# Kernel optimization log

Measured on AMD Instinct MI355X. Metric: run time of the kernel, lower is better.

The kernel has to match this reference:

```python
import jax, jax.numpy as jnp
import numpy as np

N, E, H = 1024, 2048, 32
DIMS = [4, 128, 512, 1028]
NEG_SLOPE_ATT = 0.2   # GATv2 attention LeakyReLU
NEG_SLOPE_ACT = 0.01  # torch.nn.LeakyReLU default


def _lin(key, fan_in, fan_out):
    k1, k2 = jax.random.split(key)
    s = 1.0 / np.sqrt(fan_in)
    return (jax.random.uniform(k1, (fan_in, fan_out), jnp.float32, -s, s),
            jax.random.uniform(k2, (fan_out,), jnp.float32, -s, s))


def setup_inputs() -> dict:
    key = jax.random.key(0)
    ks = jax.random.split(key, 32)
    inp = {
        'x': jax.random.normal(ks[0], (N, 4), jnp.float32),
        'edge_index': jax.random.randint(ks[1], (2, E), 0, N, jnp.int64),
    }
    # GATv2 layers: lin_l/lin_r -> heads*out, att [H, C], bias [C]
    ki = 2
    for i in range(3):
        cin, cout = DIMS[i], DIMS[i + 1]
        wl, bl = _lin(ks[ki], cin, H * cout); ki += 1
        wr, br = _lin(ks[ki], cin, H * cout); ki += 1
        att = jax.random.normal(ks[ki], (H, cout), jnp.float32) * 0.05; ki += 1
        bias = jnp.zeros((cout,), jnp.float32)
        j = i + 1
        inp.update({f'w{j}l': wl, f'b{j}l': bl, f'w{j}r': wr, f'b{j}r': br,
                    f'att{j}': att, f'gb{j}': bias})
    # decoder MLP 1028 -> 512 -> 128 -> 2
    for j, (cin, cout) in enumerate([(1028, 512), (512, 128), (128, 2)], 1):
        w, b = _lin(ks[ki], cin, cout); ki += 1
        inp[f'dw{j}'] = w
        inp[f'db{j}'] = b
    return inp


def _gatv2(x, src, dst, wl, bl, wr, br, att, bias, cout):
    # lin_l on source nodes, lin_r on target nodes (PyG GATv2Conv)
    xl = (x @ wl + bl).reshape(-1, H, cout)   # [N, H, C]
    xr = (x @ wr + br).reshape(-1, H, cout)
    e = jax.nn.leaky_relu(xl[src] + xr[dst], NEG_SLOPE_ATT)  # [Etot, H, C]
    score = jnp.einsum('ehc,hc->eh', e, att)                  # [Etot, H]
    smax = jax.ops.segment_max(score, dst, num_segments=N)
    alpha = jnp.exp(score - smax[dst])
    denom = jax.ops.segment_sum(alpha, dst, num_segments=N)
    alpha = alpha / denom[dst]
    out = jax.ops.segment_sum(alpha[:, :, None] * xl[src], dst, num_segments=N)
    return out.mean(axis=1) + bias  # concat=False: average heads


def reference(x, edge_index,
              w1l, b1l, w1r, b1r, att1, gb1,
              w2l, b2l, w2r, b2r, att2, gb2,
              w3l, b3l, w3r, b3r, att3, gb3,
              dw1, db1, dw2, db2, dw3, db3):
    # add self loops (PyG default)
    loop = jnp.arange(N, dtype=edge_index.dtype)
    src = jnp.concatenate([edge_index[0], loop])
    dst = jnp.concatenate([edge_index[1], loop])

    act = lambda z: jax.nn.leaky_relu(z, NEG_SLOPE_ACT)
    z = _gatv2(x, src, dst, w1l, b1l, w1r, b1r, att1, gb1, 128)
    z = act(z)
    z = _gatv2(z, src, dst, w2l, b2l, w2r, b2r, att2, gb2, 512)
    z = act(z)
    z = _gatv2(z, src, dst, w3l, b3l, w3r, b3r, att3, gb3, 1028)

    z = act(z @ dw1 + db1)
    z = act(z @ dw2 + db2)
    z = z @ dw3 + db3  # [N, 2]
    return z.reshape(-1)
```

## Files before the change

kernel.cpp:

```cpp
#include <hip/hip_runtime.h>
#include <cstdint>
#include <cstddef>

#define NN 1024
#define EE 2048
#define ETOT 3072
#define HH 32

typedef __bf16 bf16_t;
typedef __attribute__((ext_vector_type(8))) __bf16 bf16x8;
typedef __attribute__((ext_vector_type(4))) __bf16 bf16x4;
typedef __attribute__((ext_vector_type(2))) __bf16 bf16x2;
typedef __attribute__((ext_vector_type(4))) float f32x4;

typedef const __attribute__((address_space(1))) void gvoid_t;
typedef __attribute__((address_space(3))) void lvoid_t;

__device__ __forceinline__ void gll16(const void* g, void* l) {
    __builtin_amdgcn_global_load_lds((gvoid_t*)g, (lvoid_t*)l, 16, 0, 0);
}

__global__ void k_zero_int(int* p, int n) {
    int i = blockIdx.x * 256 + threadIdx.x;
    if (i < n) p[i] = 0;
}

__global__ void k_detect(const int* ei, int* flag) {
    int i = blockIdx.x * 256 + threadIdx.x;
    int idx = 2 * i + 1;
    if (idx < 2 * EE && ei[idx] != 0) atomicOr(flag, 1);
}

__global__ void k_edge_prep(const int* ei, const int* flag, int* srcA, int* dstA, int* cnt) {
    int e = blockIdx.x * 256 + threadIdx.x;
    if (e >= ETOT) return;
    int s, d;
    if (e < EE) {
        if (*flag) { s = ei[e]; d = ei[EE + e]; }
        else       { s = ei[2 * e]; d = ei[2 * (EE + e)]; }
        s &= (NN - 1); d &= (NN - 1);
    } else {
        s = d = e - EE;
    }
    srcA[e] = s; dstA[e] = d;
    atomicAdd(&cnt[d], 1);
}

__global__ void k_scan(const int* cnt, int* off) {
    __shared__ int sh[NN];
    int t = threadIdx.x;
    sh[t] = cnt[t];
    __syncthreads();
    for (int o = 1; o < NN; o <<= 1) {
        int v = (t >= o) ? sh[t - o] : 0;
        __syncthreads();
        sh[t] += v;
        __syncthreads();
    }
    off[t + 1] = sh[t];
    if (t == 0) off[0] = 0;
}

__global__ void k_fill(const int* dstA, const int* off, int* cur, int* csre) {
    int e = blockIdx.x * 256 + threadIdx.x;
    if (e >= ETOT) return;
    int d = dstA[e];
    int p = atomicAdd(&cur[d], 1);
    csre[off[d] + p] = e;
}

__global__ void k_convA(const float* __restrict__ A, bf16_t* __restrict__ Ab,
                        int M, int K, int Kp) {
    int idx = blockIdx.x * 256 + threadIdx.x;
    if (idx >= M * Kp) return;
    int m = idx / Kp, k = idx % Kp;
    Ab[idx] = (k < K) ? (bf16_t)A[(size_t)m * K + k] : (bf16_t)0.f;
}

__global__ void k_convB(const float* __restrict__ B, bf16_t* __restrict__ Bt,
                        int K, int Nsub, int ldb, int Kp) {
    __shared__ float sh[32][33];
    int kt = blockIdx.y * 32, nt = blockIdx.x * 32;
    int tx = threadIdx.x & 31, ty = threadIdx.x >> 5;
#pragma unroll
    for (int i = 0; i < 4; ++i) {
        int k = kt + ty + i * 8, n = nt + tx;
        sh[ty + i * 8][tx] = (k < K && n < Nsub) ? B[(size_t)k * ldb + n] : 0.f;
    }
    __syncthreads();
    int k2 = (threadIdx.x & 15) * 2;
    int nl = threadIdx.x >> 4;
#pragma unroll
    for (int i = 0; i < 2; ++i) {
        int n = nt + nl + i * 16;
        if (n < Nsub) {
            bf16x2 v;
            v[0] = (bf16_t)sh[k2][nl + i * 16];
            v[1] = (bf16_t)sh[k2 + 1][nl + i * 16];
            *(bf16x2*)(&Bt[(size_t)n * Kp + kt + k2]) = v;
        }
    }
}

__global__ __launch_bounds__(256) void k_gemm_bf16(
        const bf16_t* __restrict__ Ab, const bf16_t* __restrict__ Bt,
        const float* __restrict__ bias, void* __restrict__ Cm,
        int M, int Nsub, int Kp, int act, int obf) {
    __shared__ __align__(16) bf16_t SH[16384];
    int tid = threadIdx.x;
    int wave = tid >> 6, lane = tid & 63;
    int wm = (wave & 1) * 64, wn = (wave >> 1) * 64;
    int l16 = lane & 15, lq = lane >> 4;

    int nx = gridDim.x, ny = gridDim.y;
    int bx = blockIdx.x, by = blockIdx.y;
    int total = nx * ny;
    if ((total & 7) == 0) {
        int j = bx + nx * by;
        int w = (j & 7) * (total >> 3) + (j >> 3);
        bx = w / ny;
        by = w % ny;
    }
    int m0 = by * 128, n0 = bx * 128;

    int u0 = wave * 128 + lane;
    int u1 = u0 + 64;
    int r0 = u0 >> 2, s0 = u0 & 3;
    int r1 = u1 >> 2, s1 = u1 & 3;
    int c0 = ((s0 ^ ((r0 >> 1) & 3)) << 3);
    int c1 = ((s1 ^ ((r1 >> 1) & 3)) << 3);
    const bf16_t* gA0 = Ab + (size_t)(m0 + r0) * Kp + c0;
    const bf16_t* gA1 = Ab + (size_t)(m0 + r1) * Kp + c1;
    const bf16_t* gB0 = Bt + (size_t)(n0 + r0) * Kp + c0;
    const bf16_t* gB1 = Bt + (size_t)(n0 + r1) * Kp + c1;

    int cR = ((lq ^ ((l16 >> 1) & 3)) << 3);

    f32x4 acc[4][4] = {};
    int nt = Kp >> 5;

    {
        bf16_t* d = SH + wave * 1024;
        gll16(gA0, d); gll16(gA1, d + 512);
        gll16(gB0, d + 4096); gll16(gB1, d + 4096 + 512);
        gA0 += 32; gA1 += 32; gB0 += 32; gB1 += 32;
    }
    __syncthreads();

    for (int t = 0; t < nt; ++t) {
        int cur = t & 1;
        if (t + 1 < nt) {
            bf16_t* d = SH + (cur ^ 1) * 8192 + wave * 1024;
            gll16(gA0, d); gll16(gA1, d + 512);
            gll16(gB0, d + 4096); gll16(gB1, d + 4096 + 512);
            gA0 += 32; gA1 += 32; gB0 += 32; gB1 += 32;
        }
        __builtin_amdgcn_sched_barrier(0);
        const bf16_t* rb = SH + cur * 8192;
        bf16x8 af[4], bfr[4];
#pragma unroll
        for (int mi = 0; mi < 4; ++mi)
            af[mi] = *(const bf16x8*)(rb + (wm + mi * 16 + l16) * 32 + cR);
#pragma unroll
        for (int ni = 0; ni < 4; ++ni)
            bfr[ni] = *(const bf16x8*)(rb + 4096 + (wn + ni * 16 + l16) * 32 + cR);
#pragma unroll
        for (int mi = 0; mi < 4; ++mi)
#pragma unroll
            for (int ni = 0; ni < 4; ++ni)
                acc[mi][ni] = __builtin_amdgcn_mfma_f32_16x16x32_bf16(
                    af[mi], bfr[ni], acc[mi][ni], 0, 0, 0);
        __syncthreads();
    }

    if (obf) {
#pragma unroll
        for (int ni = 0; ni < 4; ++ni) {
            int cl = wn + ni * 16 + l16;
            float bv = bias[n0 + cl];
#pragma unroll
            for (int mi = 0; mi < 4; ++mi)
#pragma unroll
                for (int r = 0; r < 4; ++r) {
                    int rl = wm + mi * 16 + lq * 4 + r;
                    float v = acc[mi][ni][r] + bv;
                    if (act && v < 0.f) v *= 0.01f;
                    int slot = ((cl >> 3) ^ (rl & 7)) & 15;
                    SH[rl * 128 + slot * 8 + (cl & 7)] = (bf16_t)v;
                }
        }
        __syncthreads();
        bf16_t* Cb = (bf16_t*)Cm;
#pragma unroll
        for (int i = 0; i < 8; ++i) {
            int j = i * 2048 + tid * 8;
            int rl = j >> 7;
            int p = (j >> 3) & 15;
            int cl = ((p ^ (rl & 7)) & 15) * 8;
            bf16x8 v = *(const bf16x8*)(SH + rl * 128 + p * 8);
            int row = m0 + rl, col = n0 + cl;
            if (row < M) {
                if (col + 7 < Nsub) {
                    *(bf16x8*)(Cb + (size_t)row * Nsub + col) = v;
                } else {
#pragma unroll
                    for (int e = 0; e < 8; ++e)
                        if (col + e < Nsub) Cb[(size_t)row * Nsub + col + e] = v[e];
                }
            }
        }
    } else {
#pragma unroll
        for (int ni = 0; ni < 4; ++ni) {
            int col = n0 + wn + ni * 16 + l16;
            if (col >= Nsub) continue;
            float bv = bias[col];
#pragma unroll
            for (int mi = 0; mi < 4; ++mi)
#pragma unroll
                for (int r = 0; r < 4; ++r) {
                    int row = m0 + wm + mi * 16 + lq * 4 + r;
                    if (row < M) {
                        float v = acc[mi][ni][r] + bv;
                        if (act && v < 0.f) v *= 0.01f;
                        ((float*)Cm)[(size_t)row * Nsub + col] = v;
                    }
                }
        }
    }
}

#define TM 64
#define TN 64
#define TK 16
__global__ __launch_bounds__(256) void k_gemm(
        const float* __restrict__ A, const float* __restrict__ B,
        const float* __restrict__ bias, void* __restrict__ Cm,
        int M, int Nsub, int K, int ldb, int act, int obf) {
    __shared__ float As[TK][TM];
    __shared__ float Bs[TK][TN];
    int tid = threadIdx.x;
    int tx = tid % 16, ty = tid / 16;
    int m0 = blockIdx.y * TM, n0 = blockIdx.x * TN;
    float acc[4][4] = {};
    for (int k0 = 0; k0 < K; k0 += TK) {
#pragma unroll
        for (int i = 0; i < 4; ++i) {
            int idx = tid * 4 + i;
            int m = idx >> 4, k = idx & 15;
            float v = 0.f;
            if (k0 + k < K && m0 + m < M) v = A[(size_t)(m0 + m) * K + k0 + k];
            As[k][m] = v;
        }
#pragma unroll
        for (int i = 0; i < 4; ++i) {
            int idx = tid * 4 + i;
            int k = idx >> 6, n = idx & 63;
            float v = 0.f;
            if (k0 + k < K && n0 + n < Nsub) v = B[(size_t)(k0 + k) * ldb + n0 + n];
            Bs[k][n] = v;
        }
        __syncthreads();
#pragma unroll
        for (int kk = 0; kk < TK; ++kk) {
            float4 a4 = *(const float4*)&As[kk][ty * 4];
            float4 b4 = *(const float4*)&Bs[kk][tx * 4];
            float af[4] = {a4.x, a4.y, a4.z, a4.w};
            float bf[4] = {b4.x, b4.y, b4.z, b4.w};
#pragma unroll
            for (int i = 0; i < 4; ++i)
#pragma unroll
                for (int j = 0; j < 4; ++j)
                    acc[i][j] += af[i] * bf[j];
        }
        __syncthreads();
    }
#pragma unroll
    for (int i = 0; i < 4; ++i) {
        int m = m0 + ty * 4 + i;
        if (m >= M) continue;
#pragma unroll
        for (int j = 0; j < 4; ++j) {
            int n = n0 + tx * 4 + j;
            if (n < Nsub) {
                float v = acc[i][j] + bias[n];
                if (act && v < 0.f) v *= 0.01f;
                if (obf) ((bf16_t*)Cm)[(size_t)m * Nsub + n] = (bf16_t)v;
                else     ((float*)Cm)[(size_t)m * Nsub + n] = v;
            }
        }
    }
}

__global__ void k_gemm_naive(const float* __restrict__ A, const float* __restrict__ B,
                             const float* __restrict__ bias, float* __restrict__ out,
                             int M, int N, int K, int act) {
    int idx = blockIdx.x * 256 + threadIdx.x;
    if (idx >= M * N) return;
    int m = idx / N, n = idx % N;
    float s = bias[n];
    for (int k = 0; k < K; ++k)
        s += A[(size_t)m * K + k] * B[(size_t)k * N + n];
    if (act && s < 0.f) s *= 0.01f;
    out[idx] = s;
}

__global__ void k_score(const bf16_t* __restrict__ xl, const bf16_t* __restrict__ xr,
                        const float* __restrict__ att, const int* __restrict__ srcA,
                        const int* __restrict__ dstA, float* __restrict__ sc,
                        int C, int HG, int h0) {
    int wid = (blockIdx.x * 256 + threadIdx.x) >> 6;
    int lane = threadIdx.x & 63;
    if (wid >= ETOT * HG) return;
    int e = wid / HG, hl = wid % HG;
    int s = srcA[e], d = dstA[e];
    const bf16x4* pl = (const bf16x4*)(xl + ((size_t)s * HG + hl) * C);
    const bf16x4* pr = (const bf16x4*)(xr + ((size_t)d * HG + hl) * C);
    const float4* pa = (const float4*)(att + (size_t)(h0 + hl) * C);
    float acc = 0.f;
    int C4 = C >> 2;
    for (int c = lane; c < C4; c += 64) {
        bf16x4 a = pl[c], b = pr[c];
        float4 w = pa[c];
        float v;
        v = (float)a[0] + (float)b[0]; v = v > 0.f ? v : 0.2f * v; acc += v * w.x;
        v = (float)a[1] + (float)b[1]; v = v > 0.f ? v : 0.2f * v; acc += v * w.y;
        v = (float)a[2] + (float)b[2]; v = v > 0.f ? v : 0.2f * v; acc += v * w.z;
        v = (float)a[3] + (float)b[3]; v = v > 0.f ? v : 0.2f * v; acc += v * w.w;
    }
#pragma unroll
    for (int off = 32; off; off >>= 1) acc += __shfl_down(acc, off, 64);
    if (lane == 0) sc[(size_t)e * HH + h0 + hl] = acc;
}

__global__ void k_softmax(const int* __restrict__ off, const int* __restrict__ csre,
                          float* __restrict__ sc, int HG, int h0) {
    int idx = blockIdx.x * 256 + threadIdx.x;
    if (idx >= NN * HG) return;
    int d = idx / HG, h = h0 + idx % HG;
    int b = off[d], en = off[d + 1];
    float m = -1e30f;
    for (int i = b; i < en; ++i) m = fmaxf(m, sc[(size_t)csre[i] * HH + h]);
    float ssum = 0.f;
    for (int i = b; i < en; ++i) ssum += expf(sc[(size_t)csre[i] * HH + h] - m);
    float inv = 1.f / ssum;
    for (int i = b; i < en; ++i) {
        size_t p = (size_t)csre[i] * HH + h;
        sc[p] = expf(sc[p] - m) * inv;
    }
}

__global__ __launch_bounds__(256) void k_aggregate(
        const bf16_t* __restrict__ xl, const float* __restrict__ sc,
        const int* __restrict__ off, const int* __restrict__ csre,
        const int* __restrict__ srcA, const float* __restrict__ bias,
        float* __restrict__ z, int C, int HG, int h0, int lgNC,
        int first, int last, int act) {
    __shared__ float4 sh[256];
    int d = blockIdx.x;
    int NC = 1 << lgNC;
    int c4i = threadIdx.x & (NC - 1);
    int hl = threadIdx.x >> lgNC;
    int c4 = blockIdx.y * NC + c4i;
    int C4 = C >> 2;
    bool active = (c4 < C4);
    float4 acc = {0.f, 0.f, 0.f, 0.f};
    int b = off[d], en = off[d + 1];
    for (int i = b; i < en; ++i) {
        int e = csre[i];
        int s = srcA[e];
        float w = sc[(size_t)e * HH + h0 + hl];
        if (active) {
            bf16x4 vx = *((const bf16x4*)(xl + ((size_t)s * HG + hl) * C) + c4);
            acc.x += w * (float)vx[0];
            acc.y += w * (float)vx[1];
            acc.z += w * (float)vx[2];
            acc.w += w * (float)vx[3];
        }
    }
    sh[threadIdx.x] = acc;
    __syncthreads();
    for (int s = HG >> 1; s >= 1; s >>= 1) {
        if (hl < s) {
            float4 o = sh[threadIdx.x + (s << lgNC)];
            float4 m = sh[threadIdx.x];
            m.x += o.x; m.y += o.y; m.z += o.z; m.w += o.w;
            sh[threadIdx.x] = m;
        }
        __syncthreads();
    }
    if (hl == 0 && active) {
        acc = sh[threadIdx.x];
        float4* zp = (float4*)(z + (size_t)d * C) + c4;
        if (!first) {
            float4 prev = *zp;
            acc.x += prev.x; acc.y += prev.y; acc.z += prev.z; acc.w += prev.w;
        }
        if (last) {
            const float4 bz = *((const float4*)bias + c4);
            acc.x = acc.x * (1.f / 32.f) + bz.x;
            acc.y = acc.y * (1.f / 32.f) + bz.y;
            acc.z = acc.z * (1.f / 32.f) + bz.z;
            acc.w = acc.w * (1.f / 32.f) + bz.w;
            if (act) {
                acc.x = acc.x < 0.f ? acc.x * 0.01f : acc.x;
                acc.y = acc.y < 0.f ? acc.y * 0.01f : acc.y;
                acc.z = acc.z < 0.f ? acc.z * 0.01f : acc.z;
                acc.w = acc.w < 0.f ? acc.w * 0.01f : acc.w;
            }
        }
        *zp = acc;
    }
}

extern "C" void kernel_launch(void* const* d_in, const int* in_sizes, int n_in,
                              void* d_out, int out_size, void* d_ws, size_t ws_size,
                              hipStream_t stream) {
    const float* x   = (const float*)d_in[0];
    const int* ei    = (const int*)d_in[1];
    const float* w1l = (const float*)d_in[2];  const float* b1l = (const float*)d_in[3];
    const float* w1r = (const float*)d_in[4];  const float* b1r = (const float*)d_in[5];
    const float* att1= (const float*)d_in[6];  const float* gb1 = (const float*)d_in[7];
    const float* w2l = (const float*)d_in[8];  const float* b2l = (const float*)d_in[9];
    const float* w2r = (const float*)d_in[10]; const float* b2r = (const float*)d_in[11];
    const float* att2= (const float*)d_in[12]; const float* gb2 = (const float*)d_in[13];
    const float* w3l = (const float*)d_in[14]; const float* b3l = (const float*)d_in[15];
    const float* w3r = (const float*)d_in[16]; const float* b3r = (const float*)d_in[17];
    const float* att3= (const float*)d_in[18]; const float* gb3 = (const float*)d_in[19];
    const float* dw1 = (const float*)d_in[20]; const float* db1 = (const float*)d_in[21];
    const float* dw2 = (const float*)d_in[22]; const float* db2 = (const float*)d_in[23];
    const float* dw3 = (const float*)d_in[24]; const float* db3 = (const float*)d_in[25];
    float* outp = (float*)d_out;

    char* p = (char*)d_ws;
    auto alloc = [&](size_t bytes) -> char* {
        char* r = p;
        p += (bytes + 255) & ~(size_t)255;
        return r;
    };
    float* sc   = (float*)alloc((size_t)ETOT * HH * 4);
    float* za   = (float*)alloc((size_t)NN * 1028 * 4);
    float* zb   = (float*)alloc((size_t)NN * 1028 * 4);
    bf16_t* Abf = (bf16_t*)alloc((size_t)NN * 1056 * 2);
    int*   ints = (int*)  alloc((size_t)(2 * NN + 16) * 4);
    int* cnt  = ints;
    int* cur  = ints + NN;
    int* flag = ints + 2 * NN;
    int* offp = (int*)alloc((size_t)(NN + 1) * 4);
    int* csre = (int*)alloc((size_t)ETOT * 4);
    int* srcA = (int*)alloc((size_t)ETOT * 4);
    int* dstA = (int*)alloc((size_t)ETOT * 4);
    size_t used = (size_t)(p - (char*)d_ws);
    size_t remain = (ws_size > used) ? (ws_size - used) : 0;
    char* chunk = p;

    k_zero_int<<<dim3((2 * NN + 16 + 255) / 256), dim3(256), 0, stream>>>(ints, 2 * NN + 16);
    k_detect<<<dim3((EE + 255) / 256), dim3(256), 0, stream>>>(ei, flag);
    k_edge_prep<<<dim3((ETOT + 255) / 256), dim3(256), 0, stream>>>(ei, flag, srcA, dstA, cnt);
    k_scan<<<dim3(1), dim3(NN), 0, stream>>>(cnt, offp);
    k_fill<<<dim3((ETOT + 255) / 256), dim3(256), 0, stream>>>(dstA, offp, cur, csre);

    struct Layer {
        const float* in; int cin; int C;
        const float *wl, *bl, *wr, *br, *att, *gb;
        float* zout; int act;
    };
    Layer L[3] = {
        { x,    4, 128,  w1l, b1l, w1r, b1r, att1, gb1, za, 1 },
        { za, 128, 512,  w2l, b2l, w2r, b2r, att2, gb2, zb, 1 },
        { zb, 512, 1028, w3l, b3l, w3r, b3r, att3, gb3, za, 0 },
    };
    auto al = [](size_t n) { return (n + 127) & ~(size_t)127; };

    for (int li = 0; li < 3; ++li) {
        int C = L[li].C, K = L[li].cin;
        bool mfma = (K >= 128);
        int Kp = (K + 31) & ~31;
        size_t perHG = 2ull * NN * C * 2 + (mfma ? (size_t)C * Kp * 2 : 0);
        int HG = 32;
        while (HG > 1 && (size_t)HG * perHG + (1u << 20) > remain) HG >>= 1;
        int nchunk = HH / HG;
        int lgNC = 0;
        while ((1 << lgNC) * HG < 256) ++lgNC;
        int NC = 1 << lgNC;
        bf16_t* xlc = (bf16_t*)chunk;
        bf16_t* xrc = xlc + al((size_t)NN * HG * C);
        bf16_t* Bt  = xrc + al((size_t)NN * HG * C);

        if (mfma)
            k_convA<<<dim3((NN * Kp + 255) / 256), dim3(256), 0, stream>>>(L[li].in, Abf, NN, K, Kp);

        for (int hg = 0; hg < nchunk; ++hg) {
            int h0 = hg * HG;
            int colOff = h0 * C;
            int Nsub = HG * C;
            if (mfma) {
                dim3 gc((Nsub + 31) / 32, Kp / 32);
                dim3 gg((Nsub + 127) / 128, NN / 128);
                k_convB<<<gc, dim3(256), 0, stream>>>(L[li].wl + colOff, Bt, K, Nsub, HH * C, Kp);
                k_gemm_bf16<<<gg, dim3(256), 0, stream>>>(Abf, Bt, L[li].bl + colOff, xlc, NN, Nsub, Kp, 0, 1);
                k_convB<<<gc, dim3(256), 0, stream>>>(L[li].wr + colOff, Bt, K, Nsub, HH * C, Kp);
                k_gemm_bf16<<<gg, dim3(256), 0, stream>>>(Abf, Bt, L[li].br + colOff, xrc, NN, Nsub, Kp, 0, 1);
            } else {
                dim3 gg((Nsub + TN - 1) / TN, (NN + TM - 1) / TM);
                k_gemm<<<gg, dim3(256), 0, stream>>>(L[li].in, L[li].wl + colOff, L[li].bl + colOff,
                                                     xlc, NN, Nsub, K, HH * C, 0, 1);
                k_gemm<<<gg, dim3(256), 0, stream>>>(L[li].in, L[li].wr + colOff, L[li].br + colOff,
                                                     xrc, NN, Nsub, K, HH * C, 0, 1);
            }
            int waves = ETOT * HG;
            k_score<<<dim3((waves * 64 + 255) / 256), dim3(256), 0, stream>>>(
                xlc, xrc, L[li].att, srcA, dstA, sc, C, HG, h0);
            k_softmax<<<dim3((NN * HG + 255) / 256), dim3(256), 0, stream>>>(offp, csre, sc, HG, h0);
            int C4 = C >> 2;
            dim3 ga(NN, (C4 + NC - 1) / NC);
            k_aggregate<<<ga, dim3(256), 0, stream>>>(xlc, sc, offp, csre, srcA, L[li].gb,
                                                      L[li].zout, C, HG, h0, lgNC,
                                                      hg == 0, hg == nchunk - 1, L[li].act);
        }
    }

    {
        int K = 1028, Kp = 1056, Nsub = 512;
        bf16_t* Bt = (bf16_t*)chunk;
        k_convA<<<dim3((NN * Kp + 255) / 256), dim3(256), 0, stream>>>(za, Abf, NN, K, Kp);
        k_convB<<<dim3(Nsub / 32, Kp / 32), dim3(256), 0, stream>>>(dw1, Bt, K, Nsub, Nsub, Kp);
        k_gemm_bf16<<<dim3(Nsub / 128, NN / 128), dim3(256), 0, stream>>>(Abf, Bt, db1, zb, NN, Nsub, Kp, 1, 0);
    }
    k_gemm<<<dim3(128 / TN, NN / TM), dim3(256), 0, stream>>>(zb, dw2, db2, za, NN, 128, 512, 128, 1, 0);
    k_gemm_naive<<<dim3((NN * 2 + 255) / 256), dim3(256), 0, stream>>>(za, dw3, db3, outp, NN, 2, 128, 0);
}
```

Before: 748.5 us.

## Triple-buffer GEMM LDS loads with one barrier per k-step and widen B conversion stores

The bf16 GEMM main loop moves from double to triple buffering in LDS. It uses explicit vmcnt waits so two tiles of global-to-LDS loads stay in flight, and it needs only a single barrier per iteration instead of two. The B transpose/convert kernel now writes bf16x4 per thread instead of two bf16x2 stores. This adds LDS usage (48KB per block), which may reduce occupancy, and relies on hand-written waitcnt counts being correct.

```diff
diff --git a/kernel.cpp b/kernel.cpp
--- a/kernel.cpp
+++ b/kernel.cpp
@@ -88,17 +88,16 @@
         sh[ty + i * 8][tx] = (k < K && n < Nsub) ? B[(size_t)k * ldb + n] : 0.f;
     }
     __syncthreads();
-    int k2 = (threadIdx.x & 15) * 2;
-    int nl = threadIdx.x >> 4;
-#pragma unroll
-    for (int i = 0; i < 2; ++i) {
-        int n = nt + nl + i * 16;
-        if (n < Nsub) {
-            bf16x2 v;
-            v[0] = (bf16_t)sh[k2][nl + i * 16];
-            v[1] = (bf16_t)sh[k2 + 1][nl + i * 16];
-            *(bf16x2*)(&Bt[(size_t)n * Kp + kt + k2]) = v;
-        }
+    int kq = (threadIdx.x & 7) * 4;
+    int nl = threadIdx.x >> 3;
+    int n = nt + nl;
+    if (n < Nsub) {
+        bf16x4 v;
+        v[0] = (bf16_t)sh[kq][nl];
+        v[1] = (bf16_t)sh[kq + 1][nl];
+        v[2] = (bf16_t)sh[kq + 2][nl];
+        v[3] = (bf16_t)sh[kq + 3][nl];
+        *(bf16x4*)(&Bt[(size_t)n * Kp + kt + kq]) = v;
     }
 }
 
@@ -106,7 +105,7 @@
         const bf16_t* __restrict__ Ab, const bf16_t* __restrict__ Bt,
         const float* __restrict__ bias, void* __restrict__ Cm,
         int M, int Nsub, int Kp, int act, int obf) {
-    __shared__ __align__(16) bf16_t SH[16384];
+    __shared__ __align__(16) bf16_t SH[24576];
     int tid = threadIdx.x;
     int wave = tid >> 6, lane = tid & 63;
     int wm = (wave & 1) * 64, wn = (wave >> 1) * 64;
@@ -139,24 +138,29 @@
     f32x4 acc[4][4] = {};
     int nt = Kp >> 5;
 
-    {
-        bf16_t* d = SH + wave * 1024;
+#pragma unroll
+    for (int pt = 0; pt < 2; ++pt) {
+        bf16_t* d = SH + pt * 8192 + wave * 1024;
         gll16(gA0, d); gll16(gA1, d + 512);
         gll16(gB0, d + 4096); gll16(gB1, d + 4096 + 512);
         gA0 += 32; gA1 += 32; gB0 += 32; gB1 += 32;
     }
-    __syncthreads();
-
+
+    int bc = 0, bn = 2;
     for (int t = 0; t < nt; ++t) {
-        int cur = t & 1;
-        if (t + 1 < nt) {
-            bf16_t* d = SH + (cur ^ 1) * 8192 + wave * 1024;
+        if (t + 1 < nt)
+            asm volatile("s_waitcnt vmcnt(4) lgkmcnt(0)" ::: "memory");
+        else
+            asm volatile("s_waitcnt vmcnt(0) lgkmcnt(0)" ::: "memory");
+        asm volatile("s_barrier" ::: "memory");
+        __builtin_amdgcn_sched_barrier(0);
+        if (t + 2 < nt) {
+            bf16_t* d = SH + bn * 8192 + wave * 1024;
             gll16(gA0, d); gll16(gA1, d + 512);
             gll16(gB0, d + 4096); gll16(gB1, d + 4096 + 512);
             gA0 += 32; gA1 += 32; gB0 += 32; gB1 += 32;
         }
-        __builtin_amdgcn_sched_barrier(0);
-        const bf16_t* rb = SH + cur * 8192;
+        const bf16_t* rb = SH + bc * 8192;
         bf16x8 af[4], bfr[4];
 #pragma unroll
         for (int mi = 0; mi < 4; ++mi)
@@ -170,8 +174,12 @@
             for (int ni = 0; ni < 4; ++ni)
                 acc[mi][ni] = __builtin_amdgcn_mfma_f32_16x16x32_bf16(
                     af[mi], bfr[ni], acc[mi][ni], 0, 0, 0);
-        __syncthreads();
-    }
+        bc = (bc == 2) ? 0 : bc + 1;
+        bn = (bn == 2) ? 0 : bn + 1;
+    }
+    asm volatile("s_waitcnt lgkmcnt(0)" ::: "memory");
+    asm volatile("s_barrier" ::: "memory");
+    __builtin_amdgcn_sched_barrier(0);
 
     if (obf) {
 #pragma unroll
```

Result: faster. 729.8 us (-2.5%).
